# Kernel tuning notes

Measured on AMD Instinct MI355X. Metric: run time of the kernel, lower is better.

Reference implementation:

```python
import jax, jax.numpy as jnp
import numpy as np

N_EMBED = 1024
HEAD_SIZE = 64
BLOCK_SIZE = 2048

def setup_inputs() -> dict:
    key = jax.random.key(0)
    kx, kq, kk, kv = jax.random.split(key, 4)
    scale = N_EMBED ** -0.5
    x = jax.random.normal(kx, (8, 2048, N_EMBED), dtype=jnp.float32)
    # nn.Linear weights stored as [out, in]; we keep [in, out] for x @ W
    Wq = jax.random.normal(kq, (N_EMBED, HEAD_SIZE), dtype=jnp.float32) * scale
    Wk = jax.random.normal(kk, (N_EMBED, HEAD_SIZE), dtype=jnp.float32) * scale
    Wv = jax.random.normal(kv, (N_EMBED, HEAD_SIZE), dtype=jnp.float32) * scale
    return {"x": x, "Wq": Wq, "Wk": Wk, "Wv": Wv}

def reference(x, Wq, Wk, Wv):
    B, T, C = x.shape
    q = x @ Wq  # [B,T,H]
    k = x @ Wk
    v = x @ Wv
    # NOTE: original scales by C**-0.5 (n_embed), not head_size**-0.5
    wei = jnp.einsum('bth,bsh->bts', q, k) * (C ** -0.5)  # [B,T,T]
    causal = jnp.tril(jnp.ones((T, T), dtype=bool))
    wei = jnp.where(causal, wei, -jnp.inf)
    wei = jax.nn.softmax(wei, axis=-1)
    out = jnp.einsum('bts,bsh->bth', wei, v)  # [B,T,H]
    return out
```

## Files before the change

kernel.cpp:

```cpp
#include <hip/hip_runtime.h>

#define B_ 8
#define T_ 2048
#define C_ 1024
#define H_ 64

typedef __attribute__((ext_vector_type(8))) short short8;
typedef __attribute__((ext_vector_type(4))) float floatx4;
typedef __attribute__((ext_vector_type(4))) int intx4;

static __device__ __forceinline__ unsigned short f2bf(float f) {
  unsigned int u = __builtin_bit_cast(unsigned int, f);
  u += 0x7FFFu + ((u >> 16) & 1u);
  return (unsigned short)(u >> 16);
}
static __device__ __forceinline__ float bf2f(unsigned short u) {
  return __builtin_bit_cast(float, ((unsigned int)u) << 16);
}
static __device__ __forceinline__ unsigned int fbits(float f) {
  return __builtin_bit_cast(unsigned int, f);
}

typedef const __attribute__((address_space(1))) unsigned int* gp1_t;
typedef __attribute__((address_space(3))) unsigned int* lp3_t;
static __device__ __forceinline__ void gl_lds16(const void* g, void* l) {
  __builtin_amdgcn_global_load_lds((gp1_t)g, (lp3_t)l, 16, 0, 0);
}

__global__ __launch_bounds__(256) void conv_w(const float* __restrict__ wq,
    const float* __restrict__ wk, const float* __restrict__ wv,
    unsigned short* __restrict__ wt) {
  int idx = blockIdx.x * 256 + threadIdx.x;
  int mat = idx >> 14;
  int e = idx & 16383;
  int kk = e >> 4, c0 = (e & 15) * 4;
  const float* src = (mat == 0) ? wq : (mat == 1) ? wk : wv;
  float scale = (mat == 0) ? 0.03125f * 1.44269504088896340736f : 1.0f;
  float4 v = *(const float4*)&src[kk * H_ + c0];
  wt[(size_t)(mat * 64 + c0 + 0) * C_ + kk] = f2bf(v.x * scale);
  wt[(size_t)(mat * 64 + c0 + 1) * C_ + kk] = f2bf(v.y * scale);
  wt[(size_t)(mat * 64 + c0 + 2) * C_ + kk] = f2bf(v.z * scale);
  wt[(size_t)(mat * 64 + c0 + 3) * C_ + kk] = f2bf(v.w * scale);
}

__global__ __launch_bounds__(256) void qkv_proj(
    const float* __restrict__ x, const unsigned short* __restrict__ wt,
    unsigned short* __restrict__ qo, unsigned short* __restrict__ ko,
    unsigned short* __restrict__ vT) {
  __shared__ float XL[2][2048];
  __shared__ unsigned short WL[2][12288];
  int tid = threadIdx.x;
  int wave = tid >> 6, lane = tid & 63;
  int lane4 = lane & 15, quad = lane >> 4;
  int m0 = blockIdx.x * 32;

  floatx4 acc[2][3];
#pragma unroll
  for (int mt = 0; mt < 2; ++mt)
#pragma unroll
    for (int nt = 0; nt < 3; ++nt) acc[mt][nt] = (floatx4)0.0f;

#pragma unroll
  for (int j = 0; j < 2; ++j) {
    int p = (wave * 2 + j) * 64 + lane;
    int r = p >> 4, pc = p & 15;
    int cl = (pc & 8) | ((pc ^ (r & 7)) & 7);
    gl_lds16(&x[(size_t)(m0 + r) * C_ + cl * 4], &XL[0][(wave * 2 + j) * 256]);
  }
#pragma unroll
  for (int j = 0; j < 6; ++j) {
    int p = (wave * 6 + j) * 64 + lane;
    int r = p >> 3, pc = p & 7;
    int cl = pc ^ (r & 7);
    gl_lds16(&wt[(size_t)r * C_ + cl * 8], &WL[0][(wave * 6 + j) * 512]);
  }
  __syncthreads();

  for (int kt = 0; kt < 16; ++kt) {
    int buf = kt & 1;
    if (kt < 15) {
      int k0 = (kt + 1) * 64;
#pragma unroll
      for (int j = 0; j < 2; ++j) {
        int p = (wave * 2 + j) * 64 + lane;
        int r = p >> 4, pc = p & 15;
        int cl = (pc & 8) | ((pc ^ (r & 7)) & 7);
        gl_lds16(&x[(size_t)(m0 + r) * C_ + k0 + cl * 4], &XL[buf ^ 1][(wave * 2 + j) * 256]);
      }
#pragma unroll
      for (int j = 0; j < 6; ++j) {
        int p = (wave * 6 + j) * 64 + lane;
        int r = p >> 3, pc = p & 7;
        int cl = pc ^ (r & 7);
        gl_lds16(&wt[(size_t)r * C_ + k0 + cl * 8], &WL[buf ^ 1][(wave * 6 + j) * 512]);
      }
    }

#pragma unroll
    for (int ks = 0; ks < 2; ++ks) {
      short8 a[2];
#pragma unroll
      for (int mt = 0; mt < 2; ++mt) {
        int r = mt * 16 + lane4;
        int cl0 = ks * 8 + quad * 2;
        int pc0 = (cl0 & 8) | ((cl0 ^ (r & 7)) & 7);
        int pc1 = ((cl0 + 1) & 8) | (((cl0 + 1) ^ (r & 7)) & 7);
        float4 f0 = *(const float4*)&XL[buf][r * 64 + pc0 * 4];
        float4 f1 = *(const float4*)&XL[buf][r * 64 + pc1 * 4];
        intx4 pk;
        pk[0] = (int)__builtin_amdgcn_perm(fbits(f0.y), fbits(f0.x), 0x07060302u);
        pk[1] = (int)__builtin_amdgcn_perm(fbits(f0.w), fbits(f0.z), 0x07060302u);
        pk[2] = (int)__builtin_amdgcn_perm(fbits(f1.y), fbits(f1.x), 0x07060302u);
        pk[3] = (int)__builtin_amdgcn_perm(fbits(f1.w), fbits(f1.z), 0x07060302u);
        a[mt] = __builtin_bit_cast(short8, pk);
      }
      short8 b[3];
#pragma unroll
      for (int nt = 0; nt < 3; ++nt) {
        int r = (wave * 3 + nt) * 16 + lane4;
        int cl = ks * 4 + quad;
        int pc = cl ^ (r & 7);
        b[nt] = *(const short8*)&WL[buf][r * 64 + pc * 8];
      }
#pragma unroll
      for (int mt = 0; mt < 2; ++mt)
#pragma unroll
        for (int nt = 0; nt < 3; ++nt)
          acc[mt][nt] = __builtin_amdgcn_mfma_f32_16x16x32_bf16(a[mt], b[nt], acc[mt][nt], 0, 0, 0);
    }
    __syncthreads();
  }

  unsigned short* VTB = (unsigned short*)&XL[0][0];
#pragma unroll
  for (int mt = 0; mt < 2; ++mt)
#pragma unroll
    for (int nt = 0; nt < 3; ++nt) {
      int n = wave * 48 + nt * 16 + lane4;
#pragma unroll
      for (int rr = 0; rr < 4; ++rr) {
        unsigned short val = f2bf(acc[mt][nt][rr]);
        int lrow = mt * 16 + quad * 4 + rr;
        if (n < 64)       qo[(size_t)(m0 + lrow) * H_ + n] = val;
        else if (n < 128) ko[(size_t)(m0 + lrow) * H_ + n - 64] = val;
        else              VTB[(n - 128) * 40 + lrow] = val;
      }
    }
  __syncthreads();
  {
    int h = tid >> 2, ch = tid & 3;
    int batch = m0 >> 11, t0 = m0 & 2047;
    uint4 v0 = *(const uint4*)&VTB[h * 40 + ch * 8];
    *(uint4*)&vT[(size_t)(batch * 64 + h) * T_ + t0 + ch * 8] = v0;
  }
}

__global__ __launch_bounds__(256) void attn(
    const unsigned short* __restrict__ qi, const unsigned short* __restrict__ ki,
    const unsigned short* __restrict__ vT, unsigned short* __restrict__ Op,
    float* __restrict__ lsum) {
  __shared__ unsigned short KL[2][4096];
  __shared__ unsigned short VL[2][4096];
  __shared__ unsigned short PL[4][16][72];

  int tid = threadIdx.x;
  int wave = tid >> 6, lane = tid & 63;
  int lane4 = lane & 15, quad = lane >> 4;
  int qt = blockIdx.x, b = blockIdx.y, split = blockIdx.z;
  int qb = qt * 64;
  int base = b * T_;

  int ntile = qt + 1;
  int sBeg = (split * ntile) >> 2;
  int sEnd = ((split + 1) * ntile) >> 2;

  short8 aq[2];
#pragma unroll
  for (int ks = 0; ks < 2; ++ks)
    aq[ks] = *(const short8*)&qi[(size_t)(base + qb + wave * 16 + lane4) * H_ + ks * 32 + quad * 8];

  float lrow[4];
  floatx4 o[4];
#pragma unroll
  for (int r = 0; r < 4; ++r) lrow[r] = 0.0f;
#pragma unroll
  for (int nt = 0; nt < 4; ++nt) o[nt] = (floatx4)0.0f;

  int srow = lane >> 3, sc = lane & 7;

  if (sBeg < sEnd) {
    {
      int s0 = sBeg * 64;
#pragma unroll
      for (int j = 0; j < 2; ++j) {
        int r = (wave * 2 + j) * 8 + srow;
        int cl = sc ^ (r & 7);
        gl_lds16(&ki[(size_t)(base + s0 + r) * H_ + cl * 8], &KL[0][(wave * 2 + j) * 512]);
        gl_lds16(&vT[((size_t)b * H_ + r) * T_ + s0 + cl * 8], &VL[0][(wave * 2 + j) * 512]);
      }
    }
    __syncthreads();

    for (int st = sBeg; st < sEnd; ++st) {
      int bufi = (st - sBeg) & 1;
      bool hasnext = (st + 1 < sEnd);
      if (hasnext) {
        int s0 = (st + 1) * 64;
        int nb = bufi ^ 1;
#pragma unroll
        for (int j = 0; j < 2; ++j) {
          int r = (wave * 2 + j) * 8 + srow;
          int cl = sc ^ (r & 7);
          gl_lds16(&ki[(size_t)(base + s0 + r) * H_ + cl * 8], &KL[nb][(wave * 2 + j) * 512]);
          gl_lds16(&vT[((size_t)b * H_ + r) * T_ + s0 + cl * 8], &VL[nb][(wave * 2 + j) * 512]);
        }
      }

      floatx4 sacc[4];
#pragma unroll
      for (int ct = 0; ct < 4; ++ct) sacc[ct] = (floatx4)0.0f;
#pragma unroll
      for (int ks = 0; ks < 2; ++ks)
#pragma unroll
        for (int ct = 0; ct < 4; ++ct) {
          int r = ct * 16 + lane4;
          int pc = (ks * 4 + quad) ^ (r & 7);
          short8 bk = *(const short8*)&KL[bufi][r * 64 + pc * 8];
          sacc[ct] = __builtin_amdgcn_mfma_f32_16x16x32_bf16(aq[ks], bk, sacc[ct], 0, 0, 0);
        }

      if (st == qt) {
#pragma unroll
        for (int ct = 0; ct < 4; ++ct)
#pragma unroll
          for (int r = 0; r < 4; ++r) {
            int qrow = wave * 16 + quad * 4 + r;
            int scol = ct * 16 + lane4;
            if (scol > qrow) sacc[ct][r] = -3.0e38f;
          }
      }

#pragma unroll
      for (int ct = 0; ct < 4; ++ct)
#pragma unroll
        for (int r = 0; r < 4; ++r) {
          float p = exp2f(sacc[ct][r] - 8.0f);
          lrow[r] += p;
          PL[wave][quad * 4 + r][ct * 16 + lane4] = f2bf(p);
        }

#pragma unroll
      for (int ks = 0; ks < 2; ++ks) {
        short8 pa = *(const short8*)&PL[wave][lane4][ks * 32 + quad * 8];
#pragma unroll
        for (int nt = 0; nt < 4; ++nt) {
          int r = nt * 16 + lane4;
          int pc = (ks * 4 + quad) ^ (r & 7);
          short8 bv = *(const short8*)&VL[bufi][r * 64 + pc * 8];
          o[nt] = __builtin_amdgcn_mfma_f32_16x16x32_bf16(pa, bv, o[nt], 0, 0, 0);
        }
      }
      __syncthreads();
    }
  }

#pragma unroll
  for (int off = 1; off < 16; off <<= 1)
#pragma unroll
    for (int r = 0; r < 4; ++r) lrow[r] += __shfl_xor(lrow[r], off);

  size_t pbase = (((size_t)split * 8 + b) * 32 + qt) * 64;
#pragma unroll
  for (int r = 0; r < 4; ++r) {
    int row = wave * 16 + quad * 4 + r;
#pragma unroll
    for (int nt = 0; nt < 4; ++nt)
      Op[(pbase + row) * 64 + nt * 16 + lane4] = f2bf(o[nt][r]);
    if (lane4 == 0) lsum[pbase + row] = lrow[r];
  }
}

__global__ __launch_bounds__(256) void merge_splits(
    const unsigned short* __restrict__ Op, const float* __restrict__ lsum,
    float* __restrict__ out) {
  int idx = blockIdx.x * 256 + threadIdx.x;
  int row = idx >> 4;
  int h4 = (idx & 15) * 4;
  int b = row >> 11, t = row & 2047;
  int qt = t >> 6, r = t & 63;
  float O0 = 0.f, O1 = 0.f, O2 = 0.f, O3 = 0.f, l = 0.f;
#pragma unroll
  for (int s = 0; s < 4; ++s) {
    size_t p = (((size_t)s * 8 + b) * 32 + qt) * 64 + r;
    l += lsum[p];
    ushort4 ov = *(const ushort4*)&Op[p * 64 + h4];
    O0 += bf2f(ov.x); O1 += bf2f(ov.y); O2 += bf2f(ov.z); O3 += bf2f(ov.w);
  }
  float inv = 1.0f / l;
  float4 res = make_float4(O0 * inv, O1 * inv, O2 * inv, O3 * inv);
  *(float4*)&out[(size_t)row * H_ + h4] = res;
}

extern "C" void kernel_launch(void* const* d_in, const int* in_sizes, int n_in,
                              void* d_out, int out_size, void* d_ws, size_t ws_size,
                              hipStream_t stream) {
  const float* x  = (const float*)d_in[0];
  const float* wq = (const float*)d_in[1];
  const float* wk = (const float*)d_in[2];
  const float* wv = (const float*)d_in[3];
  float* out = (float*)d_out;

  char* ws = (char*)d_ws;
  unsigned short* wt = (unsigned short*)ws;
  unsigned short* qb = (unsigned short*)(ws + 393216);
  unsigned short* kb = (unsigned short*)(ws + 2490368);
  unsigned short* vt = (unsigned short*)(ws + 4587520);
  unsigned short* Op = (unsigned short*)(ws + 6684672);
  float*          ls = (float*)(ws + 15073280);

  conv_w<<<192, 256, 0, stream>>>(wq, wk, wv, wt);
  qkv_proj<<<512, 256, 0, stream>>>(x, wt, qb, kb, vt);
  attn<<<dim3(32, 8, 4), 256, 0, stream>>>(qb, kb, vt, Op, ls);
  merge_splits<<<1024, 256, 0, stream>>>(Op, ls, out);
}
```

Measured before the change: 145.9 us.

## Load K/V fragments directly from global into registers, drop LDS staging

Replaces the double-buffered global-to-LDS staging of K and V tiles, and the per-tile block barriers, with direct per-lane global loads of MFMA operand fragments into registers. It also switches the P probability conversion to bf16 from round-to-nearest to truncation. This removes LDS traffic and __syncthreads, but each wave now loads the full K/V tile itself, so L2 traffic goes up roughly fourfold and there is no explicit prefetch overlap. Truncation slightly lowers the precision of P.

```diff
diff --git a/kernel.cpp b/kernel.cpp
--- a/kernel.cpp
+++ b/kernel.cpp
@@ -13,6 +13,9 @@
   unsigned int u = __builtin_bit_cast(unsigned int, f);
   u += 0x7FFFu + ((u >> 16) & 1u);
   return (unsigned short)(u >> 16);
+}
+static __device__ __forceinline__ unsigned short f2bf_t(float f) {
+  return (unsigned short)(__builtin_bit_cast(unsigned int, f) >> 16);
 }
 static __device__ __forceinline__ float bf2f(unsigned short u) {
   return __builtin_bit_cast(float, ((unsigned int)u) << 16);
@@ -159,8 +162,6 @@
     const unsigned short* __restrict__ qi, const unsigned short* __restrict__ ki,
     const unsigned short* __restrict__ vT, unsigned short* __restrict__ Op,
     float* __restrict__ lsum) {
-  __shared__ unsigned short KL[2][4096];
-  __shared__ unsigned short VL[2][4096];
   __shared__ unsigned short PL[4][16][72];
 
   int tid = threadIdx.x;
@@ -186,81 +187,59 @@
 #pragma unroll
   for (int nt = 0; nt < 4; ++nt) o[nt] = (floatx4)0.0f;
 
-  int srow = lane >> 3, sc = lane & 7;
-
-  if (sBeg < sEnd) {
-    {
-      int s0 = sBeg * 64;
-#pragma unroll
-      for (int j = 0; j < 2; ++j) {
-        int r = (wave * 2 + j) * 8 + srow;
-        int cl = sc ^ (r & 7);
-        gl_lds16(&ki[(size_t)(base + s0 + r) * H_ + cl * 8], &KL[0][(wave * 2 + j) * 512]);
-        gl_lds16(&vT[((size_t)b * H_ + r) * T_ + s0 + cl * 8], &VL[0][(wave * 2 + j) * 512]);
-      }
-    }
-    __syncthreads();
-
-    for (int st = sBeg; st < sEnd; ++st) {
-      int bufi = (st - sBeg) & 1;
-      bool hasnext = (st + 1 < sEnd);
-      if (hasnext) {
-        int s0 = (st + 1) * 64;
-        int nb = bufi ^ 1;
-#pragma unroll
-        for (int j = 0; j < 2; ++j) {
-          int r = (wave * 2 + j) * 8 + srow;
-          int cl = sc ^ (r & 7);
-          gl_lds16(&ki[(size_t)(base + s0 + r) * H_ + cl * 8], &KL[nb][(wave * 2 + j) * 512]);
-          gl_lds16(&vT[((size_t)b * H_ + r) * T_ + s0 + cl * 8], &VL[nb][(wave * 2 + j) * 512]);
+  const unsigned short* kbase = &ki[(size_t)(base + lane4) * H_ + quad * 8];
+  const unsigned short* vbase = &vT[((size_t)b * H_ + lane4) * T_ + quad * 8];
+
+  for (int st = sBeg; st < sEnd; ++st) {
+    int s0 = st * 64;
+    short8 bk[2][4];
+#pragma unroll
+    for (int ks = 0; ks < 2; ++ks)
+#pragma unroll
+      for (int ct = 0; ct < 4; ++ct)
+        bk[ks][ct] = *(const short8*)&kbase[(size_t)(s0 + ct * 16) * H_ + ks * 32];
+    short8 bv[2][4];
+#pragma unroll
+    for (int ks = 0; ks < 2; ++ks)
+#pragma unroll
+      for (int nt = 0; nt < 4; ++nt)
+        bv[ks][nt] = *(const short8*)&vbase[(size_t)(nt * 16) * T_ + s0 + ks * 32];
+
+    floatx4 sacc[4];
+#pragma unroll
+    for (int ct = 0; ct < 4; ++ct) sacc[ct] = (floatx4)0.0f;
+#pragma unroll
+    for (int ks = 0; ks < 2; ++ks)
+#pragma unroll
+      for (int ct = 0; ct < 4; ++ct)
+        sacc[ct] = __builtin_amdgcn_mfma_f32_16x16x32_bf16(aq[ks], bk[ks][ct], sacc[ct], 0, 0, 0);
+
+    if (st == qt) {
+#pragma unroll
+      for (int ct = 0; ct < 4; ++ct)
+#pragma unroll
+        for (int r = 0; r < 4; ++r) {
+          int qrow = wave * 16 + quad * 4 + r;
+          int scol = ct * 16 + lane4;
+          if (scol > qrow) sacc[ct][r] = -3.0e38f;
         }
-      }
-
-      floatx4 sacc[4];
-#pragma unroll
-      for (int ct = 0; ct < 4; ++ct) sacc[ct] = (floatx4)0.0f;
-#pragma unroll
-      for (int ks = 0; ks < 2; ++ks)
-#pragma unroll
-        for (int ct = 0; ct < 4; ++ct) {
-          int r = ct * 16 + lane4;
-          int pc = (ks * 4 + quad) ^ (r & 7);
-          short8 bk = *(const short8*)&KL[bufi][r * 64 + pc * 8];
-          sacc[ct] = __builtin_amdgcn_mfma_f32_16x16x32_bf16(aq[ks], bk, sacc[ct], 0, 0, 0);
-        }
-
-      if (st == qt) {
-#pragma unroll
-        for (int ct = 0; ct < 4; ++ct)
-#pragma unroll
-          for (int r = 0; r < 4; ++r) {
-            int qrow = wave * 16 + quad * 4 + r;
-            int scol = ct * 16 + lane4;
-            if (scol > qrow) sacc[ct][r] = -3.0e38f;
-          }
-      }
-
-#pragma unroll
-      for (int ct = 0; ct < 4; ++ct)
-#pragma unroll
-        for (int r = 0; r < 4; ++r) {
-          float p = exp2f(sacc[ct][r] - 8.0f);
-          lrow[r] += p;
-          PL[wave][quad * 4 + r][ct * 16 + lane4] = f2bf(p);
-        }
-
-#pragma unroll
-      for (int ks = 0; ks < 2; ++ks) {
-        short8 pa = *(const short8*)&PL[wave][lane4][ks * 32 + quad * 8];
-#pragma unroll
-        for (int nt = 0; nt < 4; ++nt) {
-          int r = nt * 16 + lane4;
-          int pc = (ks * 4 + quad) ^ (r & 7);
-          short8 bv = *(const short8*)&VL[bufi][r * 64 + pc * 8];
-          o[nt] = __builtin_amdgcn_mfma_f32_16x16x32_bf16(pa, bv, o[nt], 0, 0, 0);
-        }
-      }
-      __syncthreads();
+    }
+
+#pragma unroll
+    for (int ct = 0; ct < 4; ++ct)
+#pragma unroll
+      for (int r = 0; r < 4; ++r) {
+        float p = exp2f(sacc[ct][r] - 8.0f);
+        lrow[r] += p;
+        PL[wave][quad * 4 + r][ct * 16 + lane4] = f2bf_t(p);
+      }
+
+#pragma unroll
+    for (int ks = 0; ks < 2; ++ks) {
+      short8 pa = *(const short8*)&PL[wave][lane4][ks * 32 + quad * 8];
+#pragma unroll
+      for (int nt = 0; nt < 4; ++nt)
+        o[nt] = __builtin_amdgcn_mfma_f32_16x16x32_bf16(pa, bv[ks][nt], o[nt], 0, 0, 0);
     }
   }
 
```

After: 176.4 us. 20.8% more time.
